# Kernel tuning notes

Measured on AMD Instinct MI355X. Metric: run time of the kernel, lower is better.

Reference implementation:

```python
import jax, jax.numpy as jnp
import numpy as np

B, S, E, H = 2, 2048, 1024, 16
D = E // H

def setup_inputs() -> dict:
    key = jax.random.key(0)
    ks = jax.random.split(key, 9)
    s = 1.0 / np.sqrt(E)
    return {
        "x": jax.random.normal(ks[0], (B, S, E), dtype=jnp.float32),
        "mask": jnp.ones((B, S), dtype=bool),
        "Wq_w": jax.random.normal(ks[1], (E, E), dtype=jnp.float32) * s,
        "Wq_b": jax.random.normal(ks[2], (E,), dtype=jnp.float32) * s,
        "Wk_w": jax.random.normal(ks[3], (E, E), dtype=jnp.float32) * s,
        "Wk_b": jax.random.normal(ks[4], (E,), dtype=jnp.float32) * s,
        "Wv_w": jax.random.normal(ks[5], (E, E), dtype=jnp.float32) * s,
        "Wv_b": jax.random.normal(ks[6], (E,), dtype=jnp.float32) * s,
        "Wo_w": jax.random.normal(ks[7], (E, E), dtype=jnp.float32) * s,
        "Wo_b": jax.random.normal(ks[8], (E,), dtype=jnp.float32) * s,
    }

def _split_heads(t):
    # [B,S,E] -> [B,H,S,D]
    return t.reshape(B, S, H, D).transpose(0, 2, 1, 3)

def reference(x, mask, Wq_w, Wq_b, Wk_w, Wk_b, Wv_w, Wv_b, Wo_w, Wo_b):
    # torch nn.Linear: y = x @ W.T + b
    q = _split_heads(x @ Wq_w.T + Wq_b)
    k = _split_heads(x @ Wk_w.T + Wk_b)
    v = _split_heads(x @ Wv_w.T + Wv_b)
    scores = jnp.einsum("bhqd,bhkd->bhqk", q, k) / jnp.sqrt(jnp.float32(D))
    # key-padding mask [B,S] -> broadcast over heads and query positions
    m = mask[:, None, None, :]  # [B,1,1,S]
    scores = jnp.where(m, scores, jnp.float32(-jnp.inf))
    probs = jax.nn.softmax(scores, axis=-1)
    attn = jnp.einsum("bhqk,bhkd->bhqd", probs, v)  # [B,H,S,D]
    attn = attn.transpose(0, 2, 1, 3).reshape(B, S, E)
    return attn @ Wo_w.T + Wo_b
```

## Files before the change

kernel.cpp:

```cpp
#include <hip/hip_runtime.h>
#include <hip/hip_bf16.h>
#include <stdint.h>
#include <stddef.h>

#define Bb 2
#define Ss 2048
#define Ee 1024
#define Hh 16
#define Dd 64
#define BH (Bb * Hh)

typedef __attribute__((ext_vector_type(8))) short short8;
typedef __attribute__((ext_vector_type(8))) __bf16 bf16x8;
typedef __attribute__((ext_vector_type(4))) float f32x4;
typedef __attribute__((ext_vector_type(4))) unsigned int u32x4;

__device__ __forceinline__ short f2bf(float f) {
  union { float f; uint32_t u; } c;
  c.f = f;
  uint32_t u = c.u;
  return (short)((u + 0x7FFFu + ((u >> 16) & 1u)) >> 16);
}
__device__ __forceinline__ f32x4 mfma_bf16(short8 a, short8 b, f32x4 c) {
  return __builtin_amdgcn_mfma_f32_16x16x32_bf16(
      __builtin_bit_cast(bf16x8, a), __builtin_bit_cast(bf16x8, b), c, 0, 0, 0);
}
__device__ __forceinline__ short8 load8cvt(const float* p) {
  const f32x4 a = *(const f32x4*)p;
  const f32x4 b = *(const f32x4*)(p + 4);
  short8 r;
  r[0] = f2bf(a[0]); r[1] = f2bf(a[1]); r[2] = f2bf(a[2]); r[3] = f2bf(a[3]);
  r[4] = f2bf(b[0]); r[5] = f2bf(b[1]); r[6] = f2bf(b[2]); r[7] = f2bf(b[3]);
  return r;
}

__device__ __forceinline__ void glds16(const short* g, short* l) {
  __builtin_amdgcn_global_load_lds(
      (const __attribute__((address_space(1))) void*)g,
      (__attribute__((address_space(3))) void*)l, 16, 0, 0);
}

__device__ __forceinline__ unsigned cvt_pk_bf16(float lo, float hi) {
  unsigned r;
  asm("v_cvt_pk_bf16_f32 %0, %1, %2" : "=v"(r) : "v"(lo), "v"(hi));
  return r;
}

__device__ __forceinline__ void xpose4(unsigned a, unsigned b,
                                       unsigned& lo, unsigned& hi) {
  asm("v_permlane32_swap_b32 %0, %1" : "+v"(a), "+v"(b));
  asm("v_permlane16_swap_b32 %0, %1" : "+v"(a), "+v"(b));
  lo = a; hi = b;
}

__global__ __launch_bounds__(256) void cvt_all(
    const float* __restrict__ x,  const float* __restrict__ wk,
    const float* __restrict__ wv, const float* __restrict__ wo,
    const float* __restrict__ wq, short* __restrict__ xb,
    short* __restrict__ wkb, short* __restrict__ wvb,
    short* __restrict__ wob, short* __restrict__ wqb) {
  const int blk = blockIdx.x;
  const float* src; short* dst; size_t base;
  if (blk < 2048)      { src = x;  dst = xb;  base = (size_t)blk * 2048; }
  else if (blk < 2560) { src = wk; dst = wkb; base = (size_t)(blk - 2048) * 2048; }
  else if (blk < 3072) { src = wv; dst = wvb; base = (size_t)(blk - 2560) * 2048; }
  else if (blk < 3584) { src = wo; dst = wob; base = (size_t)(blk - 3072) * 2048; }
  else                 { src = wq; dst = wqb; base = (size_t)(blk - 3584) * 2048; }
  const size_t off = base + (size_t)threadIdx.x * 8;
  *(short8*)&dst[off] = load8cvt(&src[off]);
}

__global__ __launch_bounds__(512) void gemm_kv(
    const short* __restrict__ xbf, const short* __restrict__ Wk,
    const short* __restrict__ Wv, const float* __restrict__ bk,
    const float* __restrict__ bv, short* __restrict__ outK,
    short* __restrict__ outVt) {
  __shared__ __align__(16) short As[2][8192];
  __shared__ __align__(16) short Bs[2][8192];
  const int tid = threadIdx.x;
  const int lane = tid & 63, wave = tid >> 6;
  const int lrow = lane & 15, quad = lane >> 4;
  const int lin = blockIdx.x + 32 * blockIdx.y;
  const int cls = lin & 7, idx = lin >> 3;
  const int bx = 8 * (cls & 3) + (idx & 7);
  const int by = 8 * (cls >> 2) + (idx >> 3);
  const int isV = by >> 3;
  const int m0 = isV ? (by & 7) * 128 : bx * 128;
  const int n0 = isV ? bx * 128 : (by & 7) * 128;
  const short* Ap = isV ? Wv : xbf;
  const short* Bp = isV ? xbf : Wk;
  const int wm = (wave >> 2) * 64, wn = (wave & 3) * 32;

  f32x4 acc[4][2];
#pragma unroll
  for (int i = 0; i < 4; ++i)
#pragma unroll
    for (int j = 0; j < 2; ++j) acc[i][j] = {0.f, 0.f, 0.f, 0.f};

  auto stage = [&](int k0, int bi) {
#pragma unroll
    for (int t = 0; t < 2; ++t) {
      const int p = tid + t * 512;
      const int r = p >> 3, g = (p & 7) ^ (r & 7);
      glds16(&Ap[(size_t)(m0 + r) * Ee + k0 + g * 8], &As[bi][p * 8]);
      glds16(&Bp[(size_t)(n0 + r) * Ee + k0 + g * 8], &Bs[bi][p * 8]);
    }
  };
  stage(0, 0);
  __syncthreads();
  for (int it = 0; it < Ee / 64; ++it) {
    const int bi = it & 1;
    if (it + 1 < Ee / 64) stage((it + 1) * 64, bi ^ 1);
#pragma unroll
    for (int c2 = 0; c2 < 2; ++c2) {
      const int sA = ((c2 * 4 + quad) ^ (lrow & 7)) * 8;
      short8 af[4], bfr[2];
#pragma unroll
      for (int i = 0; i < 4; ++i)
        af[i] = *(short8*)&As[bi][(wm + i * 16 + lrow) * 64 + sA];
#pragma unroll
      for (int j = 0; j < 2; ++j)
        bfr[j] = *(short8*)&Bs[bi][(wn + j * 16 + lrow) * 64 + sA];
#pragma unroll
      for (int i = 0; i < 4; ++i)
#pragma unroll
        for (int j = 0; j < 2; ++j)
          acc[i][j] = mfma_bf16(af[i], bfr[j], acc[i][j]);
    }
    __syncthreads();
  }

  if (isV) {
#pragma unroll
    for (int i = 0; i < 4; ++i) {
#pragma unroll
      for (int r = 0; r < 4; ++r) {
        const int m = m0 + wm + i * 16 + quad * 4 + r;
        const int h = m >> 6, d = m & 63;
        const float bv_ = bv[m];
#pragma unroll
        for (int j = 0; j < 2; ++j) {
          const int n = n0 + wn + j * 16 + lrow;
          const int b = n >> 11, s = n & 2047;
          outVt[((size_t)(b * Hh + h) * Dd + d) * Ss + s] =
              f2bf(acc[i][j][r] + bv_);
        }
      }
    }
  } else {
#pragma unroll
    for (int j = 0; j < 2; ++j) {
      const int n = n0 + wn + j * 16 + lrow;
      const float bk_ = bk[n];
      const int h = n >> 6, d = n & 63;
#pragma unroll
      for (int i = 0; i < 4; ++i) {
#pragma unroll
        for (int r = 0; r < 4; ++r) {
          const int m = m0 + wm + i * 16 + quad * 4 + r;
          const int b = m >> 11, s = m & 2047;
          outK[((size_t)(b * Hh + h) * Ss + s) * Dd + d] =
              f2bf(acc[i][j][r] + bk_);
        }
      }
    }
  }
}

__global__ __launch_bounds__(512) void gemm_out(
    const short* __restrict__ A, const short* __restrict__ Bt,
    const float* __restrict__ bias, float* __restrict__ out) {
  __shared__ __align__(16) short As[2][4096];
  __shared__ __align__(16) short Bs[2][8192];
  const int tid = threadIdx.x;
  const int lane = tid & 63, wave = tid >> 6;
  const int lrow = lane & 15, quad = lane >> 4;
  const int m0 = blockIdx.x * 64, n0 = blockIdx.y * 128;
  const int wm = (wave >> 2) * 32, wn = (wave & 3) * 32;

  f32x4 acc[2][2];
#pragma unroll
  for (int i = 0; i < 2; ++i)
#pragma unroll
    for (int j = 0; j < 2; ++j) acc[i][j] = {0.f, 0.f, 0.f, 0.f};

  auto stage = [&](int k0, int bi) {
    {
      const int r = tid >> 3, g = (tid & 7) ^ (r & 7);
      glds16(&A[(size_t)(m0 + r) * Ee + k0 + g * 8], &As[bi][tid * 8]);
    }
#pragma unroll
    for (int t = 0; t < 2; ++t) {
      const int p = tid + t * 512;
      const int r = p >> 3, g = (p & 7) ^ (r & 7);
      glds16(&Bt[(size_t)(n0 + r) * Ee + k0 + g * 8], &Bs[bi][p * 8]);
    }
  };
  stage(0, 0);
  __syncthreads();
  for (int it = 0; it < Ee / 64; ++it) {
    const int bi = it & 1;
    if (it + 1 < Ee / 64) stage((it + 1) * 64, bi ^ 1);
#pragma unroll
    for (int c2 = 0; c2 < 2; ++c2) {
      const int sA = ((c2 * 4 + quad) ^ (lrow & 7)) * 8;
      short8 af[2], bfr[2];
#pragma unroll
      for (int i = 0; i < 2; ++i)
        af[i] = *(short8*)&As[bi][(wm + i * 16 + lrow) * 64 + sA];
#pragma unroll
      for (int j = 0; j < 2; ++j)
        bfr[j] = *(short8*)&Bs[bi][(wn + j * 16 + lrow) * 64 + sA];
#pragma unroll
      for (int i = 0; i < 2; ++i)
#pragma unroll
        for (int j = 0; j < 2; ++j)
          acc[i][j] = mfma_bf16(af[i], bfr[j], acc[i][j]);
    }
    __syncthreads();
  }

#pragma unroll
  for (int j = 0; j < 2; ++j) {
    const int n = n0 + wn + j * 16 + lrow;
    const float bv = bias[n];
#pragma unroll
    for (int i = 0; i < 2; ++i)
#pragma unroll
      for (int r = 0; r < 4; ++r) {
        const int m = m0 + wm + i * 16 + quad * 4 + r;
        out[(size_t)m * Ee + n] = acc[i][j][r] + bv;
      }
  }
}

__global__ __launch_bounds__(512, 4) void attn_fused(
    const short* __restrict__ xbf, const short* __restrict__ Wqb,
    const float* __restrict__ Wq_b, const short* __restrict__ Kd,
    const short* __restrict__ Vt, short* __restrict__ outA) {
  __shared__ __align__(16) short smem[32768];
  const int tid = threadIdx.x, lane = tid & 63, wave = tid >> 6;
  const int lrow = lane & 15, quad = lane >> 4;
  const int half = wave >> 2, wq = wave & 3;
  const int bh = blockIdx.x, b = bh >> 4, h = bh & 15;
  const int qt = blockIdx.y;

  const short* kp = Kd + (size_t)bh * Ss * Dd;
  const short* vp = Vt + (size_t)bh * Dd * Ss;

  const int keyg = tid >> 3, jg = (tid & 7) ^ (keyg & 7);
  const short* klo = kp + keyg * Dd + jg * 8;
  const short* khi = kp + (1024 + keyg) * Dd + jg * 8;
  const short* vlo = vp + (size_t)keyg * Ss + jg * 8;
  const short* vhi = vp + (size_t)keyg * Ss + 1024 + jg * 8;
  const int ldst = tid * 8;

  auto stagePair = [&](short* base) {
    glds16(klo, base + ldst);
    glds16(vlo, base + 4096 + ldst);
    glds16(khi, base + 8192 + ldst);
    glds16(vhi, base + 12288 + ldst);
    klo += 64 * Dd; khi += 64 * Dd;
    vlo += 64; vhi += 64;
  };

  auto stageQ = [&](int kc, int qi) {
    short* xq = smem + qi * 12288;
#pragma unroll
    for (int t = 0; t < 2; ++t) {
      const int p = tid + t * 512;
      const int r = p >> 3, g = (p & 7) ^ (r & 7);
      glds16(&xbf[((size_t)b * Ss + qt * 128 + r) * Ee + kc * 64 + g * 8],
             &xq[p * 8]);
    }
    {
      const int r = tid >> 3, g = (tid & 7) ^ (r & 7);
      glds16(&Wqb[(size_t)(h * 64 + r) * Ee + kc * 64 + g * 8],
             &xq[8192 + tid * 8]);
    }
  };

  f32x4 qacc[4];
#pragma unroll
  for (int dt = 0; dt < 4; ++dt) qacc[dt] = {0.f, 0.f, 0.f, 0.f};
  stageQ(0, 0);
  __syncthreads();
  for (int kc = 0; kc < Ee / 64; ++kc) {
    const int qi = kc & 1;
    if (kc + 1 < Ee / 64) stageQ(kc + 1, qi ^ 1);
    const short* xq = smem + qi * 12288;
    const short* wqp = xq + 8192;
#pragma unroll
    for (int c2 = 0; c2 < 2; ++c2) {
      const int sA = ((c2 * 4 + quad) ^ (lrow & 7)) * 8;
      const short8 xf = *(short8*)&xq[(wave * 16 + lrow) * 64 + sA];
#pragma unroll
      for (int dt = 0; dt < 4; ++dt) {
        const short8 wf = *(short8*)&wqp[(dt * 16 + lrow) * 64 + sA];
        qacc[dt] = mfma_bf16(wf, xf, qacc[dt]);
      }
    }
    __syncthreads();
  }

  short8 qf[2];
  {
    const float sc = 0.125f * 1.4426950408889634f;
    unsigned c0[4], c1[4];
#pragma unroll
    for (int dt = 0; dt < 4; ++dt) {
      const f32x4 bq = *(const f32x4*)&Wq_b[h * 64 + dt * 16 + quad * 4];
      c0[dt] = cvt_pk_bf16((qacc[dt][0] + bq[0]) * sc,
                           (qacc[dt][1] + bq[1]) * sc);
      c1[dt] = cvt_pk_bf16((qacc[dt][2] + bq[2]) * sc,
                           (qacc[dt][3] + bq[3]) * sc);
    }
    unsigned e0, e1, e2, e3;
    xpose4(c0[0], c0[1], e0, e2);
    xpose4(c1[0], c1[1], e1, e3);
    { u32x4 t = {e0, e1, e2, e3}; qf[0] = __builtin_bit_cast(short8, t); }
    xpose4(c0[2], c0[3], e0, e2);
    xpose4(c1[2], c1[3], e1, e3);
    { u32x4 t = {e0, e1, e2, e3}; qf[1] = __builtin_bit_cast(short8, t); }
  }

  short* Ql = smem + 24576;
  *(short8*)&Ql[(wave * 16 + lrow) * 64 + ((quad) ^ (lrow & 7)) * 8] = qf[0];
  *(short8*)&Ql[(wave * 16 + lrow) * 64 + ((4 + quad) ^ (lrow & 7)) * 8] = qf[1];
  stagePair(smem);
  asm volatile("s_waitcnt lgkmcnt(0)" ::: "memory");
  __builtin_amdgcn_s_barrier();

  short8 qfA[2], qfB[2];
  {
    const int qa = wq * 32 + lrow, qb = qa + 16;
    qfA[0] = *(short8*)&Ql[qa * 64 + ((quad) ^ (lrow & 7)) * 8];
    qfA[1] = *(short8*)&Ql[qa * 64 + ((4 + quad) ^ (lrow & 7)) * 8];
    qfB[0] = *(short8*)&Ql[qb * 64 + ((quad) ^ (lrow & 7)) * 8];
    qfB[1] = *(short8*)&Ql[qb * 64 + ((4 + quad) ^ (lrow & 7)) * 8];
  }

  f32x4 occA[4], occB[4], occLA, occLB;
#pragma unroll
  for (int dt = 0; dt < 4; ++dt) {
    occA[dt] = {0.f, 0.f, 0.f, 0.f};
    occB[dt] = {0.f, 0.f, 0.f, 0.f};
  }
  occLA = {0.f, 0.f, 0.f, 0.f};
  occLB = {0.f, 0.f, 0.f, 0.f};

  const u32x4 onesu = {0x3F803F80u, 0x3F803F80u, 0x3F803F80u, 0x3F803F80u};
  const short8 onesb = __builtin_bit_cast(short8, onesu);

  const int sw0 = ((quad) ^ (lrow & 7)) * 8;
  const int sw1 = ((4 + quad) ^ (lrow & 7)) * 8;
  const int krow = lrow * 64;

  for (int r = 0; r < Ss / 128; ++r) {
    asm volatile("s_waitcnt vmcnt(0)" ::: "memory");
    __builtin_amdgcn_s_barrier();
    if (r + 1 < Ss / 128) stagePair(smem + ((r + 1) & 1) * 16384);
    const short* cur = smem + (r & 1) * 16384 + half * 8192;

    f32x4 stA[4], stB[4];
    __builtin_amdgcn_s_setprio(1);
#pragma unroll
    for (int kk = 0; kk < 4; ++kk) {
      stA[kk] = {0.f, 0.f, 0.f, 0.f};
      stB[kk] = {0.f, 0.f, 0.f, 0.f};
      const short8 k0 = *(short8*)&cur[kk * 1024 + krow + sw0];
      const short8 k1 = *(short8*)&cur[kk * 1024 + krow + sw1];
      stA[kk] = mfma_bf16(k0, qfA[0], stA[kk]);
      stA[kk] = mfma_bf16(k1, qfA[1], stA[kk]);
      stB[kk] = mfma_bf16(k0, qfB[0], stB[kk]);
      stB[kk] = mfma_bf16(k1, qfB[1], stB[kk]);
    }
    __builtin_amdgcn_s_setprio(0);

    short8 paA0, paA1, paB0, paB1;
    {
      unsigned c0[4], c1[4];
#pragma unroll
      for (int kk = 0; kk < 4; ++kk) {
        c0[kk] = cvt_pk_bf16(__builtin_amdgcn_exp2f(stA[kk][0]),
                             __builtin_amdgcn_exp2f(stA[kk][1]));
        c1[kk] = cvt_pk_bf16(__builtin_amdgcn_exp2f(stA[kk][2]),
                             __builtin_amdgcn_exp2f(stA[kk][3]));
      }
      unsigned e0, e1, e2, e3;
      xpose4(c0[0], c0[1], e0, e2);
      xpose4(c1[0], c1[1], e1, e3);
      { u32x4 t = {e0, e1, e2, e3}; paA0 = __builtin_bit_cast(short8, t); }
      xpose4(c0[2], c0[3], e0, e2);
      xpose4(c1[2], c1[3], e1, e3);
      { u32x4 t = {e0, e1, e2, e3}; paA1 = __builtin_bit_cast(short8, t); }
    }
    {
      unsigned c0[4], c1[4];
#pragma unroll
      for (int kk = 0; kk < 4; ++kk) {
        c0[kk] = cvt_pk_bf16(__builtin_amdgcn_exp2f(stB[kk][0]),
                             __builtin_amdgcn_exp2f(stB[kk][1]));
        c1[kk] = cvt_pk_bf16(__builtin_amdgcn_exp2f(stB[kk][2]),
                             __builtin_amdgcn_exp2f(stB[kk][3]));
      }
      unsigned e0, e1, e2, e3;
      xpose4(c0[0], c0[1], e0, e2);
      xpose4(c1[0], c1[1], e1, e3);
      { u32x4 t = {e0, e1, e2, e3}; paB0 = __builtin_bit_cast(short8, t); }
      xpose4(c0[2], c0[3], e0, e2);
      xpose4(c1[2], c1[3], e1, e3);
      { u32x4 t = {e0, e1, e2, e3}; paB1 = __builtin_bit_cast(short8, t); }
    }

    __builtin_amdgcn_s_setprio(1);
    occLA = mfma_bf16(paA0, onesb, occLA);
    occLA = mfma_bf16(paA1, onesb, occLA);
    occLB = mfma_bf16(paB0, onesb, occLB);
    occLB = mfma_bf16(paB1, onesb, occLB);
#pragma unroll
    for (int dt = 0; dt < 4; ++dt) {
      const short8 v0 = *(short8*)&cur[4096 + dt * 1024 + krow + sw0];
      const short8 v1 = *(short8*)&cur[4096 + dt * 1024 + krow + sw1];
      occA[dt] = mfma_bf16(paA0, v0, occA[dt]);
      occA[dt] = mfma_bf16(paA1, v1, occA[dt]);
      occB[dt] = mfma_bf16(paB0, v0, occB[dt]);
      occB[dt] = mfma_bf16(paB1, v1, occB[dt]);
    }
    __builtin_amdgcn_s_setprio(0);
  }

  __syncthreads();
  float* C = (float*)smem;
  const int slot = (wq * 64 + lane) * 44;
  if (half) {
#pragma unroll
    for (int dt = 0; dt < 4; ++dt) {
      *(f32x4*)&C[slot + dt * 4] = occA[dt];
      *(f32x4*)&C[slot + 16 + dt * 4] = occB[dt];
    }
    *(f32x4*)&C[slot + 32] = occLA;
    *(f32x4*)&C[slot + 36] = occLB;
  }
  __syncthreads();
  if (!half) {
#pragma unroll
    for (int dt = 0; dt < 4; ++dt) {
      occA[dt] += *(const f32x4*)&C[slot + dt * 4];
      occB[dt] += *(const f32x4*)&C[slot + 16 + dt * 4];
    }
    occLA += *(const f32x4*)&C[slot + 32];
    occLB += *(const f32x4*)&C[slot + 36];

    float invA[4], invB[4];
#pragma unroll
    for (int r = 0; r < 4; ++r) {
      invA[r] = 1.f / occLA[r];
      invB[r] = 1.f / occLB[r];
    }
#pragma unroll
    for (int dt = 0; dt < 4; ++dt)
#pragma unroll
      for (int r = 0; r < 4; ++r) {
        const int sA_ = qt * 128 + wq * 32 + quad * 4 + r;
        const int sB_ = sA_ + 16;
        outA[((size_t)b * Ss + sA_) * Ee + h * Dd + dt * 16 + lrow] =
            f2bf(occA[dt][r] * invA[r]);
        outA[((size_t)b * Ss + sB_) * Ee + h * Dd + dt * 16 + lrow] =
            f2bf(occB[dt][r] * invB[r]);
      }
  }
}

extern "C" void kernel_launch(void* const* d_in, const int* in_sizes, int n_in,
                              void* d_out, int out_size, void* d_ws, size_t ws_size,
                              hipStream_t stream) {
  (void)in_sizes; (void)n_in; (void)out_size; (void)ws_size;
  const float* x    = (const float*)d_in[0];
  const float* Wq_w = (const float*)d_in[2];
  const float* Wq_b = (const float*)d_in[3];
  const float* Wk_w = (const float*)d_in[4];
  const float* Wk_b = (const float*)d_in[5];
  const float* Wv_w = (const float*)d_in[6];
  const float* Wv_b = (const float*)d_in[7];
  const float* Wo_w = (const float*)d_in[8];
  const float* Wo_b = (const float*)d_in[9];
  float* out = (float*)d_out;

  const size_t nElem = (size_t)Bb * Ss * Ee;
  const size_t nW = (size_t)Ee * Ee;
  short* Vtws = (short*)d_ws;
  short* Aws  = Vtws + nElem;
  short* Wkb  = Aws + nElem;
  short* Wvb  = Wkb + nW;
  short* Wob  = Wvb + nW;
  short* Wqb  = Wob + nW;
  short* Kws = (short*)d_out;
  short* xbf = (short*)d_out + nElem;

  cvt_all<<<dim3(4096), dim3(256), 0, stream>>>(x, Wk_w, Wv_w, Wo_w, Wq_w,
                                                xbf, Wkb, Wvb, Wob, Wqb);
  gemm_kv<<<dim3(32, 16), dim3(512), 0, stream>>>(xbf, Wkb, Wvb, Wk_b, Wv_b,
                                                  Kws, Vtws);
  attn_fused<<<dim3(BH, Ss / 128), dim3(512), 0, stream>>>(xbf, Wqb, Wq_b, Kws,
                                                           Vtws, Aws);
  gemm_out<<<dim3(64, 8), dim3(512), 0, stream>>>(Aws, Wob, Wo_b, out);
}
```

Before: 178.8 us.

## Enlarge gemm_kv tiles to 256x128 with triple-buffered async LDS pipeline

gemm_kv now computes 256x128 output tiles per block instead of 128x128, which halves the grid to 256 blocks, and each wave produces a 64x64 sub-tile. The single shared buffer is split three ways so two k-stages are in flight, synchronised with an explicit vmcnt wait plus barrier instead of __syncthreads after every iteration. The block-index swizzle is reworked for the new grid. This should give more reuse per loaded tile and hide global-load latency better, at the cost of 144KB of LDS and more accumulator registers, which limits occupancy to one block per CU.

```diff
diff --git a/kernel.cpp b/kernel.cpp
--- a/kernel.cpp
+++ b/kernel.cpp
@@ -75,60 +75,87 @@
     const short* __restrict__ Wv, const float* __restrict__ bk,
     const float* __restrict__ bv, short* __restrict__ outK,
     short* __restrict__ outVt) {
-  __shared__ __align__(16) short As[2][8192];
-  __shared__ __align__(16) short Bs[2][8192];
+  __shared__ __align__(16) short smem[73728];
   const int tid = threadIdx.x;
   const int lane = tid & 63, wave = tid >> 6;
   const int lrow = lane & 15, quad = lane >> 4;
-  const int lin = blockIdx.x + 32 * blockIdx.y;
-  const int cls = lin & 7, idx = lin >> 3;
-  const int bx = 8 * (cls & 3) + (idx & 7);
-  const int by = 8 * (cls >> 2) + (idx >> 3);
+  const int lin = blockIdx.x + 16 * blockIdx.y;
+  const int swz = (lin & 7) * 32 + (lin >> 3);
+  const int bx = swz & 15, by = swz >> 4;
   const int isV = by >> 3;
-  const int m0 = isV ? (by & 7) * 128 : bx * 128;
-  const int n0 = isV ? bx * 128 : (by & 7) * 128;
+  const int vsub = by & 7;
+  const int m0 = isV ? (vsub & 3) * 256 : bx * 256;
+  const int n0 = isV ? (bx + (vsub >> 2) * 16) * 128 : (by & 7) * 128;
   const short* Ap = isV ? Wv : xbf;
   const short* Bp = isV ? xbf : Wk;
-  const int wm = (wave >> 2) * 64, wn = (wave & 3) * 32;
-
-  f32x4 acc[4][2];
+  const int wm = (wave >> 1) * 64, wn = (wave & 1) * 64;
+
+  const short* ap[4];
+  const short* bp[2];
+  int adst[4], bdst[2];
+#pragma unroll
+  for (int t = 0; t < 4; ++t) {
+    const int p = tid + t * 512;
+    const int r = p >> 3, g = (p & 7) ^ (r & 7);
+    ap[t] = &Ap[(size_t)(m0 + r) * Ee + g * 8];
+    adst[t] = p * 8;
+  }
+#pragma unroll
+  for (int t = 0; t < 2; ++t) {
+    const int p = tid + t * 512;
+    const int r = p >> 3, g = (p & 7) ^ (r & 7);
+    bp[t] = &Bp[(size_t)(n0 + r) * Ee + g * 8];
+    bdst[t] = 16384 + p * 8;
+  }
+  auto stage = [&](short* buf) {
+#pragma unroll
+    for (int t = 0; t < 4; ++t) { glds16(ap[t], buf + adst[t]); ap[t] += 64; }
+#pragma unroll
+    for (int t = 0; t < 2; ++t) { glds16(bp[t], buf + bdst[t]); bp[t] += 64; }
+  };
+
+  f32x4 acc[4][4];
 #pragma unroll
   for (int i = 0; i < 4; ++i)
 #pragma unroll
-    for (int j = 0; j < 2; ++j) acc[i][j] = {0.f, 0.f, 0.f, 0.f};
-
-  auto stage = [&](int k0, int bi) {
-#pragma unroll
-    for (int t = 0; t < 2; ++t) {
-      const int p = tid + t * 512;
-      const int r = p >> 3, g = (p & 7) ^ (r & 7);
-      glds16(&Ap[(size_t)(m0 + r) * Ee + k0 + g * 8], &As[bi][p * 8]);
-      glds16(&Bp[(size_t)(n0 + r) * Ee + k0 + g * 8], &Bs[bi][p * 8]);
-    }
-  };
-  stage(0, 0);
-  __syncthreads();
-  for (int it = 0; it < Ee / 64; ++it) {
-    const int bi = it & 1;
-    if (it + 1 < Ee / 64) stage((it + 1) * 64, bi ^ 1);
+    for (int j = 0; j < 4; ++j) acc[i][j] = {0.f, 0.f, 0.f, 0.f};
+
+  short* s0 = smem;
+  short* s1 = smem + 24576;
+  short* s2 = smem + 49152;
+
+  stage(s0);
+  stage(s1);
+
+  auto compute = [&](const short* buf) {
 #pragma unroll
     for (int c2 = 0; c2 < 2; ++c2) {
       const int sA = ((c2 * 4 + quad) ^ (lrow & 7)) * 8;
-      short8 af[4], bfr[2];
+      short8 af[4], bfr[4];
 #pragma unroll
       for (int i = 0; i < 4; ++i)
-        af[i] = *(short8*)&As[bi][(wm + i * 16 + lrow) * 64 + sA];
-#pragma unroll
-      for (int j = 0; j < 2; ++j)
-        bfr[j] = *(short8*)&Bs[bi][(wn + j * 16 + lrow) * 64 + sA];
+        af[i] = *(short8*)&buf[(wm + i * 16 + lrow) * 64 + sA];
+#pragma unroll
+      for (int j = 0; j < 4; ++j)
+        bfr[j] = *(short8*)&buf[16384 + (wn + j * 16 + lrow) * 64 + sA];
 #pragma unroll
       for (int i = 0; i < 4; ++i)
 #pragma unroll
-        for (int j = 0; j < 2; ++j)
+        for (int j = 0; j < 4; ++j)
           acc[i][j] = mfma_bf16(af[i], bfr[j], acc[i][j]);
     }
-    __syncthreads();
-  }
+  };
+
+  for (int it = 0; it < Ee / 64 - 1; ++it) {
+    asm volatile("s_waitcnt vmcnt(6)" ::: "memory");
+    __builtin_amdgcn_s_barrier();
+    if (it + 2 < Ee / 64) stage(s2);
+    compute(s0);
+    short* t = s0; s0 = s1; s1 = s2; s2 = t;
+  }
+  asm volatile("s_waitcnt vmcnt(0)" ::: "memory");
+  __builtin_amdgcn_s_barrier();
+  compute(s0);
 
   if (isV) {
 #pragma unroll
@@ -139,7 +166,7 @@
         const int h = m >> 6, d = m & 63;
         const float bv_ = bv[m];
 #pragma unroll
-        for (int j = 0; j < 2; ++j) {
+        for (int j = 0; j < 4; ++j) {
           const int n = n0 + wn + j * 16 + lrow;
           const int b = n >> 11, s = n & 2047;
           outVt[((size_t)(b * Hh + h) * Dd + d) * Ss + s] =
@@ -149,7 +176,7 @@
     }
   } else {
 #pragma unroll
-    for (int j = 0; j < 2; ++j) {
+    for (int j = 0; j < 4; ++j) {
       const int n = n0 + wn + j * 16 + lrow;
       const float bk_ = bk[n];
       const int h = n >> 6, d = n & 63;
@@ -500,7 +527,7 @@
 
   cvt_all<<<dim3(4096), dim3(256), 0, stream>>>(x, Wk_w, Wv_w, Wo_w, Wq_w,
                                                 xbf, Wkb, Wvb, Wob, Wqb);
-  gemm_kv<<<dim3(32, 16), dim3(512), 0, stream>>>(xbf, Wkb, Wvb, Wk_b, Wv_b,
+  gemm_kv<<<dim3(16, 16), dim3(512), 0, stream>>>(xbf, Wkb, Wvb, Wk_b, Wv_b,
                                                   Kws, Vtws);
   attn_fused<<<dim3(BH, Ss / 128), dim3(512), 0, stream>>>(xbf, Wqb, Wq_b, Kws,
                                                            Vtws, Aws);
```

After: 180.2 us, median of 2. No clear change (+0.8%).
